# Performance work log

Hardware: AMD Instinct MI355X
Metric: run time of the kernel (lower is better)

The kernel has to match this reference:

```python
import jax, jax.numpy as jnp
import numpy as np

N = 50000
E = 800000
F_IN = 128
H = 128
M = 256


def setup_inputs() -> dict:
    key = jax.random.key(0)
    ks = jax.random.split(key, 12)
    x = jax.random.normal(ks[0], (N, F_IN), dtype=jnp.float32)
    edge_index = jax.random.randint(ks[1], (2, E), 0, N, dtype=jnp.int64)

    def glorot(k, shape):
        fan_in, fan_out = shape
        s = jnp.sqrt(6.0 / (fan_in + fan_out)).astype(jnp.float32)
        return jax.random.uniform(k, shape, jnp.float32, -s, s)

    return {
        "x": x,
        "edge_index": edge_index,
        # SAGEConv1: lin_l (neighbor aggregate, with bias), lin_r (root, no bias)
        "W1l": glorot(ks[2], (F_IN, H)), "b1l": jnp.zeros((H,), jnp.float32),
        "W1r": glorot(ks[3], (F_IN, H)),
        # SAGEConv2
        "W2l": glorot(ks[4], (H, H)), "b2l": jnp.zeros((H,), jnp.float32),
        "W2r": glorot(ks[5], (H, H)),
        # edge MLP: Linear(2H -> M), ReLU, Linear(M -> 1)
        "W3": glorot(ks[6], (2 * H, M)), "b3": jnp.zeros((M,), jnp.float32),
        "W4": glorot(ks[7], (M, 1)), "b4": jnp.zeros((1,), jnp.float32),
    }


def _sage_conv(x, src, dst, Wl, bl, Wr, num_nodes):
    # mean aggregation of source-node features at destination nodes
    agg = jax.ops.segment_sum(x[src], dst, num_segments=num_nodes)  # [N, F]
    cnt = jax.ops.segment_sum(jnp.ones((src.shape[0],), x.dtype), dst,
                              num_segments=num_nodes)
    agg = agg / jnp.maximum(cnt, 1.0)[:, None]
    # out = lin_l(agg) + lin_r(x)
    return agg @ Wl + bl + x @ Wr


def reference(x, edge_index, W1l, b1l, W1r, W2l, b2l, W2r, W3, b3, W4, b4):
    src, dst = edge_index[0], edge_index[1]
    h = jax.nn.relu(_sage_conv(x, src, dst, W1l, b1l, W1r, N))   # dropout: eval mode, identity
    h = jax.nn.relu(_sage_conv(h, src, dst, W2l, b2l, W2r, N))
    edge_feat = jnp.concatenate([h[src], h[dst]], axis=-1)       # [E, 2H]
    hidden = jax.nn.relu(edge_feat @ W3 + b3)                    # [E, M]
    pred = hidden @ W4 + b4                                      # [E, 1]
    return pred.reshape(-1)
```

## Files before the change

kernel.cpp:

```cpp
#include <hip/hip_runtime.h>
#include <hip/hip_bf16.h>

#define NN 50000
#define NE 800000
#define SCAN_G ((NN + 255) / 256)

typedef __attribute__((ext_vector_type(8))) short short8;
typedef __attribute__((ext_vector_type(4))) float f32x4;

__device__ inline float bf_lo(unsigned u) { u <<= 16; float f; __builtin_memcpy(&f, &u, 4); return f; }
__device__ inline float bf_hi(unsigned u) { u &= 0xffff0000u; float f; __builtin_memcpy(&f, &u, 4); return f; }
__device__ inline unsigned pack_bf16x2(float a, float b) {
    __hip_bfloat16 ba = __float2bfloat16(a), bb = __float2bfloat16(b);
    unsigned short ua, ub;
    __builtin_memcpy(&ua, &ba, 2);
    __builtin_memcpy(&ub, &bb, 2);
    return (unsigned)ua | ((unsigned)ub << 16);
}
__device__ inline __hip_bfloat16 f2bf(float a) { return __float2bfloat16(a); }

__global__ __launch_bounds__(256) void prep_all(const float* __restrict__ W3,
                                                __hip_bfloat16* __restrict__ wpq,
                                                const float* __restrict__ W1l,
                                                const float* __restrict__ W1r,
                                                const float* __restrict__ W2l,
                                                const float* __restrict__ W2r,
                                                __hip_bfloat16* __restrict__ w12t,
                                                int* __restrict__ cnt) {
    const int b = blockIdx.x;
    if (b < SCAN_G) {
        const int i = b * 256 + threadIdx.x;
        if (i < NN) cnt[i] = 0;
    } else if (b < SCAN_G + 64) {
        const int idx4 = ((b - SCAN_G) * 256 + threadIdx.x) * 4;
        const int c = idx4 >> 7;
        const int k0 = idx4 & 127;
#pragma unroll
        for (int i = 0; i < 4; ++i) {
            const int k = k0 + i;
            const float v = (c < 256) ? W3[k * 256 + c] : W3[(128 + k) * 256 + (c - 256)];
            wpq[c * 128 + k] = __float2bfloat16(v);
        }
    } else {
        const int idx = (b - SCAN_G - 64) * 256 + threadIdx.x;
        const int layer = idx >> 15;
        const int c = (idx >> 7) & 255;
        const int k = idx & 127;
        const float* W = layer ? (c < 128 ? W2l : W2r) : (c < 128 ? W1l : W1r);
        w12t[idx] = __float2bfloat16(W[k * 128 + (c & 127)]);
    }
}

__global__ __launch_bounds__(256) void hist_kernel(const int* __restrict__ ei,
                                                   int* __restrict__ cnt) {
    for (int e = blockIdx.x * 256 + threadIdx.x; e < NE; e += gridDim.x * 256)
        atomicAdd(&cnt[ei[NE + e]], 1);
}

__global__ __launch_bounds__(256) void scan_blk(const int* __restrict__ cnt,
                                                int* __restrict__ off,
                                                int* __restrict__ bsum) {
    __shared__ int sm[256];
    const int t = threadIdx.x;
    const int i = blockIdx.x * 256 + t;
    const int v = (i < NN) ? cnt[i] : 0;
    sm[t] = v;
    __syncthreads();
    for (int d = 1; d < 256; d <<= 1) {
        const int add = (t >= d) ? sm[t - d] : 0;
        __syncthreads();
        sm[t] += add;
        __syncthreads();
    }
    if (i < NN) off[i] = sm[t] - v;
    if (t == 255) bsum[blockIdx.x] = sm[255];
}

__global__ __launch_bounds__(256) void scan_add(int* __restrict__ off,
                                                int* __restrict__ cursor,
                                                const int* __restrict__ bsum) {
    __shared__ int red[256];
    const int t = threadIdx.x;
    int s = 0;
    for (int j = t; j < blockIdx.x; j += 256) s += bsum[j];
    red[t] = s;
    __syncthreads();
    for (int d = 128; d; d >>= 1) {
        if (t < d) red[t] += red[t + d];
        __syncthreads();
    }
    const int base = red[0];
    const int i = blockIdx.x * 256 + t;
    if (i < NN) {
        const int v = off[i] + base;
        off[i] = v;
        cursor[i] = v;
    }
    if (i == NN - 1) off[NN] = NE;
}

__global__ __launch_bounds__(256) void fill_kernel(const int* __restrict__ ei,
                                                   int* __restrict__ cursor,
                                                   int* __restrict__ ssrc,
                                                   int2* __restrict__ sde) {
    for (int e = blockIdx.x * 256 + threadIdx.x; e < NE; e += gridDim.x * 256) {
        const int d = ei[NE + e];
        const int p = atomicAdd(&cursor[d], 1);
        ssrc[p] = ei[e];
        sde[p] = make_int2(d, e);
    }
}

template <bool IN_F32>
__global__ __launch_bounds__(256) void proj_gemm(const void* __restrict__ inp,
                                                 const __hip_bfloat16* __restrict__ wt,
                                                 __hip_bfloat16* __restrict__ ob) {
    __shared__ __align__(16) char A[16384];
    const int t = threadIdx.x;
    const int n0 = blockIdx.x * 64;
    {
        const int row = t >> 2, part = t & 3;
        const int node = n0 + row;
        const int sw = (row & 7) << 4;
        if (IN_F32) {
            const float* xp = (const float*)inp + (size_t)node * 128 + part * 32;
#pragma unroll
            for (int i = 0; i < 8; ++i) {
                uint2 w = make_uint2(0u, 0u);
                if (node < NN) {
                    const float4 v = *(const float4*)(xp + i * 4);
                    w.x = pack_bf16x2(v.x, v.y);
                    w.y = pack_bf16x2(v.z, v.w);
                }
                const int inner = part * 64 + i * 8;
                *(uint2*)(A + row * 256 + (inner ^ sw)) = w;
            }
        } else {
            const char* srcp = (const char*)((const __hip_bfloat16*)inp + (size_t)node * 128);
#pragma unroll
            for (int i = 0; i < 4; ++i) {
                const int inner = part * 64 + i * 16;
                uint4 v = make_uint4(0u, 0u, 0u, 0u);
                if (node < NN) v = *(const uint4*)(srcp + inner);
                *(uint4*)(A + row * 256 + (inner ^ sw)) = v;
            }
        }
    }
    __syncthreads();

    const int w = t >> 6, l = t & 63;
    const int lr = l & 15, lg = l >> 4;
    const int cb = w * 64;
    f32x4 acc[4][4] = {};
    for (int ks = 0; ks < 4; ++ks) {
        short8 af[4], bf[4];
        const int innerA = ks * 64 + lg * 16;
#pragma unroll
        for (int rt = 0; rt < 4; ++rt) {
            const int row = rt * 16 + lr;
            af[rt] = *(const short8*)(A + row * 256 + (innerA ^ ((row & 7) << 4)));
        }
        const int kidx = ks * 32 + lg * 8;
#pragma unroll
        for (int ct = 0; ct < 4; ++ct) {
            const int col = cb + ct * 16 + lr;
            bf[ct] = *(const short8*)(wt + col * 128 + kidx);
        }
#pragma unroll
        for (int rt = 0; rt < 4; ++rt)
#pragma unroll
            for (int ct = 0; ct < 4; ++ct)
                acc[rt][ct] = __builtin_amdgcn_mfma_f32_16x16x32_bf16(af[rt], bf[ct], acc[rt][ct], 0, 0, 0);
    }
#pragma unroll
    for (int rt = 0; rt < 4; ++rt) {
        __syncthreads();
#pragma unroll
        for (int ct = 0; ct < 4; ++ct) {
            const int col = cb + ct * 16 + lr;
#pragma unroll
            for (int j = 0; j < 4; ++j) {
                const int row = lg * 4 + j;
                *(__hip_bfloat16*)(A + row * 528 + col * 2) = f2bf(acc[rt][ct][j]);
            }
        }
        __syncthreads();
        const int row = t >> 4, cc = t & 15;
        const int node = n0 + rt * 16 + row;
        if (node < NN) {
#pragma unroll
            for (int pass = 0; pass < 2; ++pass) {
                const int byteoff = pass * 256 + cc * 16;
                *(uint4*)((char*)(ob + (size_t)node * 256) + byteoff) =
                    *(const uint4*)(A + row * 528 + byteoff);
            }
        }
    }
}

__global__ __launch_bounds__(256) void gather_fuse(const __hip_bfloat16* __restrict__ ob,
                                                   const int* __restrict__ off,
                                                   const int* __restrict__ ssrc,
                                                   const float* __restrict__ bl,
                                                   __hip_bfloat16* __restrict__ outp) {
    const int wv = threadIdx.x >> 6, lane = threadIdx.x & 63;
    const float2 bv = *(const float2*)&bl[lane * 2];
    for (int n = blockIdx.x * 4 + wv; n < NN; n += gridDim.x * 4) {
        const int b = off[n], e = off[n + 1];
        float a0 = 0.f, a1 = 0.f;
        int i = b;
        int s0 = (i + 0 < e) ? ssrc[i + 0] : 0;
        int s1 = (i + 1 < e) ? ssrc[i + 1] : 0;
        int s2 = (i + 2 < e) ? ssrc[i + 2] : 0;
        int s3 = (i + 3 < e) ? ssrc[i + 3] : 0;
        for (; i + 4 <= e;) {
            const unsigned u0 = *(const unsigned*)(ob + (size_t)s0 * 256 + lane * 2);
            const unsigned u1 = *(const unsigned*)(ob + (size_t)s1 * 256 + lane * 2);
            const unsigned u2 = *(const unsigned*)(ob + (size_t)s2 * 256 + lane * 2);
            const unsigned u3 = *(const unsigned*)(ob + (size_t)s3 * 256 + lane * 2);
            i += 4;
            s0 = (i + 0 < e) ? ssrc[i + 0] : 0;
            s1 = (i + 1 < e) ? ssrc[i + 1] : 0;
            s2 = (i + 2 < e) ? ssrc[i + 2] : 0;
            s3 = (i + 3 < e) ? ssrc[i + 3] : 0;
            a0 += bf_lo(u0) + bf_lo(u1) + bf_lo(u2) + bf_lo(u3);
            a1 += bf_hi(u0) + bf_hi(u1) + bf_hi(u2) + bf_hi(u3);
        }
        if (i < e) {
            const unsigned u = *(const unsigned*)(ob + (size_t)s0 * 256 + lane * 2);
            a0 += bf_lo(u); a1 += bf_hi(u); ++i;
            if (i < e) {
                const unsigned u1_ = *(const unsigned*)(ob + (size_t)s1 * 256 + lane * 2);
                a0 += bf_lo(u1_); a1 += bf_hi(u1_); ++i;
                if (i < e) {
                    const unsigned u2_ = *(const unsigned*)(ob + (size_t)s2 * 256 + lane * 2);
                    a0 += bf_lo(u2_); a1 += bf_hi(u2_);
                }
            }
        }
        const float inv = 1.0f / fmaxf((float)(e - b), 1.0f);
        const unsigned uz = *(const unsigned*)(ob + (size_t)n * 256 + 128 + lane * 2);
        const float h0 = fmaxf(a0 * inv + bf_lo(uz) + bv.x, 0.0f);
        const float h1 = fmaxf(a1 * inv + bf_hi(uz) + bv.y, 0.0f);
        *(unsigned*)((char*)outp + (size_t)n * 256 + lane * 4) = pack_bf16x2(h0, h1);
    }
}

__global__ __launch_bounds__(256) void pq_gemm(const __hip_bfloat16* __restrict__ h2b,
                                               const __hip_bfloat16* __restrict__ wpq,
                                               const float* __restrict__ b3,
                                               __hip_bfloat16* __restrict__ pqb) {
    __shared__ __align__(16) char A[16640];
    const int t = threadIdx.x;
    const int n0 = blockIdx.x * 64;
    {
        const int row = t >> 2, part = t & 3;
        const int node = n0 + row;
        const int sw = (row & 7) << 4;
#pragma unroll
        for (int i = 0; i < 4; ++i) {
            const int inner = part * 64 + i * 16;
            uint4 v = make_uint4(0u, 0u, 0u, 0u);
            if (node < NN) v = *(const uint4*)((const char*)(h2b + node * 128) + inner);
            *(uint4*)(A + row * 256 + (inner ^ sw)) = v;
        }
    }
    __syncthreads();

    const int w = t >> 6, l = t & 63;
    const int lr = l & 15, lg = l >> 4;
    const int cb = w * 128;
    f32x4 acc[4][8] = {};
    for (int ks = 0; ks < 4; ++ks) {
        short8 af[4], bf[8];
        const int innerA = ks * 64 + lg * 16;
#pragma unroll
        for (int rt = 0; rt < 4; ++rt) {
            const int row = rt * 16 + lr;
            af[rt] = *(const short8*)(A + row * 256 + (innerA ^ ((row & 7) << 4)));
        }
        const int kidx = ks * 32 + lg * 8;
#pragma unroll
        for (int ct = 0; ct < 8; ++ct) {
            const int col = cb + ct * 16 + lr;
            bf[ct] = *(const short8*)(wpq + col * 128 + kidx);
        }
#pragma unroll
        for (int rt = 0; rt < 4; ++rt)
#pragma unroll
            for (int ct = 0; ct < 8; ++ct)
                acc[rt][ct] = __builtin_amdgcn_mfma_f32_16x16x32_bf16(af[rt], bf[ct], acc[rt][ct], 0, 0, 0);
    }
    float badd[8];
#pragma unroll
    for (int ct = 0; ct < 8; ++ct) {
        const int col = cb + ct * 16 + lr;
        badd[ct] = (col >= 256) ? b3[col - 256] : 0.f;
    }
#pragma unroll
    for (int rt = 0; rt < 4; ++rt) {
        __syncthreads();
#pragma unroll
        for (int ct = 0; ct < 8; ++ct) {
            const int col = cb + ct * 16 + lr;
#pragma unroll
            for (int j = 0; j < 4; ++j) {
                const int row = lg * 4 + j;
                *(__hip_bfloat16*)(A + row * 1040 + col * 2) = f2bf(acc[rt][ct][j] + badd[ct]);
            }
        }
        __syncthreads();
        const int row = t >> 4, cc = t & 15;
        const int node = n0 + rt * 16 + row;
        if (node < NN) {
#pragma unroll
            for (int pass = 0; pass < 4; ++pass) {
                const int byteoff = pass * 256 + cc * 16;
                *(uint4*)((char*)(pqb + (size_t)node * 512) + byteoff) =
                    *(const uint4*)(A + row * 1040 + byteoff);
            }
        }
    }
}

__global__ __launch_bounds__(256) void edge_kernel(const int* __restrict__ ssrc,
                                                   const int2* __restrict__ sde,
                                                   const __hip_bfloat16* __restrict__ pqb,
                                                   const float* __restrict__ W4,
                                                   const float* __restrict__ b4,
                                                   float* __restrict__ out) {
    const int i = threadIdx.x & 7;
    const int g = threadIdx.x >> 3;
    float w4r[4][8];
#pragma unroll
    for (int j = 0; j < 4; ++j)
#pragma unroll
        for (int u = 0; u < 8; ++u)
            w4r[j][u] = W4[i * 8 + j * 64 + u];
    const float b4v = b4[0];
    for (int p = blockIdx.x * 64 + g * 2; p < NE; p += gridDim.x * 64) {
        const int s0 = ssrc[p], s1 = ssrc[p + 1];
        const int2 de0 = sde[p], de1 = sde[p + 1];
        const char* P0 = (const char*)(pqb + (size_t)s0 * 512 + i * 8);
        const char* Q0 = (const char*)(pqb + (size_t)de0.x * 512 + 256 + i * 8);
        const char* P1 = (const char*)(pqb + (size_t)s1 * 512 + i * 8);
        const char* Q1 = (const char*)(pqb + (size_t)de1.x * 512 + 256 + i * 8);
        uint4 pv0[4], qv0[4], pv1[4], qv1[4];
#pragma unroll
        for (int j = 0; j < 4; ++j) {
            pv0[j] = *(const uint4*)(P0 + j * 128);
            qv0[j] = *(const uint4*)(Q0 + j * 128);
            pv1[j] = *(const uint4*)(P1 + j * 128);
            qv1[j] = *(const uint4*)(Q1 + j * 128);
        }
        float acc0 = 0.f, acc1 = 0.f;
#pragma unroll
        for (int j = 0; j < 4; ++j) {
            const unsigned pa0[4] = {pv0[j].x, pv0[j].y, pv0[j].z, pv0[j].w};
            const unsigned qa0[4] = {qv0[j].x, qv0[j].y, qv0[j].z, qv0[j].w};
            const unsigned pa1[4] = {pv1[j].x, pv1[j].y, pv1[j].z, pv1[j].w};
            const unsigned qa1[4] = {qv1[j].x, qv1[j].y, qv1[j].z, qv1[j].w};
#pragma unroll
            for (int q4 = 0; q4 < 4; ++q4) {
                const float h0l = fmaxf(bf_lo(pa0[q4]) + bf_lo(qa0[q4]), 0.f);
                const float h0h = fmaxf(bf_hi(pa0[q4]) + bf_hi(qa0[q4]), 0.f);
                acc0 = fmaf(h0l, w4r[j][q4 * 2], acc0);
                acc0 = fmaf(h0h, w4r[j][q4 * 2 + 1], acc0);
                const float h1l = fmaxf(bf_lo(pa1[q4]) + bf_lo(qa1[q4]), 0.f);
                const float h1h = fmaxf(bf_hi(pa1[q4]) + bf_hi(qa1[q4]), 0.f);
                acc1 = fmaf(h1l, w4r[j][q4 * 2], acc1);
                acc1 = fmaf(h1h, w4r[j][q4 * 2 + 1], acc1);
            }
        }
#pragma unroll
        for (int m = 1; m <= 4; m <<= 1) {
            acc0 += __shfl_xor(acc0, m);
            acc1 += __shfl_xor(acc1, m);
        }
        if (i == 0) {
            out[de0.y] = acc0 + b4v;
            out[de1.y] = acc1 + b4v;
        }
    }
}

extern "C" void kernel_launch(void* const* d_in, const int* in_sizes, int n_in,
                              void* d_out, int out_size, void* d_ws, size_t ws_size,
                              hipStream_t stream) {
    const float* x   = (const float*)d_in[0];
    const int* ei    = (const int*)d_in[1];
    const float* W1l = (const float*)d_in[2];
    const float* b1l = (const float*)d_in[3];
    const float* W1r = (const float*)d_in[4];
    const float* W2l = (const float*)d_in[5];
    const float* b2l = (const float*)d_in[6];
    const float* W2r = (const float*)d_in[7];
    const float* W3  = (const float*)d_in[8];
    const float* b3  = (const float*)d_in[9];
    const float* W4  = (const float*)d_in[10];
    const float* b4  = (const float*)d_in[11];
    float* out = (float*)d_out;

    char* ws = (char*)d_ws;
    int* cnt            = (int*)(ws);
    int* off            = (int*)(ws + 200704);
    int* cursor         = (int*)(ws + 401408);
    int* bsum           = cursor + NN;
    int* ssrc           = (int*)(ws + 602112);
    int2* sde           = (int2*)(ws + 3802112);
    __hip_bfloat16* pqb = (__hip_bfloat16*)(ws + 10202112);
    __hip_bfloat16* h1b = (__hip_bfloat16*)(ws + 23002112);
    __hip_bfloat16* ob  = (__hip_bfloat16*)(ws + 35802112);
    __hip_bfloat16* h2b = (__hip_bfloat16*)(ws + 61402112);
    __hip_bfloat16* wpq = (__hip_bfloat16*)(ws + 74202112);
    __hip_bfloat16* w12t= (__hip_bfloat16*)(ws + 74333184);

    prep_all<<<SCAN_G + 64 + 256, 256, 0, stream>>>(W3, wpq, W1l, W1r, W2l, W2r, w12t, cnt);
    hist_kernel<<<1024, 256, 0, stream>>>(ei, cnt);
    scan_blk<<<SCAN_G, 256, 0, stream>>>(cnt, off, bsum);
    scan_add<<<SCAN_G, 256, 0, stream>>>(off, cursor, bsum);
    fill_kernel<<<1024, 256, 0, stream>>>(ei, cursor, ssrc, sde);

    proj_gemm<true><<<(NN + 63) / 64, 256, 0, stream>>>((const void*)x, w12t, ob);
    gather_fuse<<<2048, 256, 0, stream>>>(ob, off, ssrc, b1l, h1b);
    proj_gemm<false><<<(NN + 63) / 64, 256, 0, stream>>>((const void*)h1b, w12t + 256 * 128, ob);
    gather_fuse<<<2048, 256, 0, stream>>>(ob, off, ssrc, b2l, h2b);
    pq_gemm<<<(NN + 63) / 64, 256, 0, stream>>>(h2b, wpq, b3, pqb);
    edge_kernel<<<2048, 256, 0, stream>>>(ssrc, sde, pqb, W4, b4, out);
}
```

Baseline: 396.2 us.

## Fuse layer-1 neighbor gather with layer-2 projection GEMM

Adds a fused kernel that performs the mean-aggregation gather, bias, root add and ReLU for layer 1, writes the resulting bf16 rows directly into shared memory, and then runs the layer-2 projection MFMA GEMM in the same block. This removes the h1 intermediate write and read and one kernel launch. In exchange the gather now runs with only 782 blocks of 64 nodes each instead of a grid-stride 2048-block launch, which may reduce latency hiding for the irregular gathers. Workspace buffers are re-assigned, and pqb aliases ob1, which is safe because ob1 is dead by then.

Measured after the change: 441.5 us. 11.4% more time.

```diff
diff --git a/kernel.cpp b/kernel.cpp
--- a/kernel.cpp
+++ b/kernel.cpp
@@ -111,8 +111,7 @@
     }
 }
 
-template <bool IN_F32>
-__global__ __launch_bounds__(256) void proj_gemm(const void* __restrict__ inp,
+__global__ __launch_bounds__(256) void proj_gemm(const float* __restrict__ inp,
                                                  const __hip_bfloat16* __restrict__ wt,
                                                  __hip_bfloat16* __restrict__ ob) {
     __shared__ __align__(16) char A[16384];
@@ -122,28 +121,17 @@
         const int row = t >> 2, part = t & 3;
         const int node = n0 + row;
         const int sw = (row & 7) << 4;
-        if (IN_F32) {
-            const float* xp = (const float*)inp + (size_t)node * 128 + part * 32;
-#pragma unroll
-            for (int i = 0; i < 8; ++i) {
-                uint2 w = make_uint2(0u, 0u);
-                if (node < NN) {
-                    const float4 v = *(const float4*)(xp + i * 4);
-                    w.x = pack_bf16x2(v.x, v.y);
-                    w.y = pack_bf16x2(v.z, v.w);
-                }
-                const int inner = part * 64 + i * 8;
-                *(uint2*)(A + row * 256 + (inner ^ sw)) = w;
-            }
-        } else {
-            const char* srcp = (const char*)((const __hip_bfloat16*)inp + (size_t)node * 128);
-#pragma unroll
-            for (int i = 0; i < 4; ++i) {
-                const int inner = part * 64 + i * 16;
-                uint4 v = make_uint4(0u, 0u, 0u, 0u);
-                if (node < NN) v = *(const uint4*)(srcp + inner);
-                *(uint4*)(A + row * 256 + (inner ^ sw)) = v;
-            }
+        const float* xp = inp + (size_t)node * 128 + part * 32;
+#pragma unroll
+        for (int i = 0; i < 8; ++i) {
+            uint2 w = make_uint2(0u, 0u);
+            if (node < NN) {
+                const float4 v = *(const float4*)(xp + i * 4);
+                w.x = pack_bf16x2(v.x, v.y);
+                w.y = pack_bf16x2(v.z, v.w);
+            }
+            const int inner = part * 64 + i * 8;
+            *(uint2*)(A + row * 256 + (inner ^ sw)) = w;
         }
     }
     __syncthreads();
@@ -192,6 +180,115 @@
             for (int pass = 0; pass < 2; ++pass) {
                 const int byteoff = pass * 256 + cc * 16;
                 *(uint4*)((char*)(ob + (size_t)node * 256) + byteoff) =
+                    *(const uint4*)(A + row * 528 + byteoff);
+            }
+        }
+    }
+}
+
+__global__ __launch_bounds__(256) void fused_gp(const __hip_bfloat16* __restrict__ ob_in,
+                                                const int* __restrict__ off,
+                                                const int* __restrict__ ssrc,
+                                                const float* __restrict__ bl,
+                                                const __hip_bfloat16* __restrict__ wt,
+                                                __hip_bfloat16* __restrict__ ob_out) {
+    __shared__ __align__(16) char A[16384];
+    const int t = threadIdx.x;
+    const int n0 = blockIdx.x * 64;
+    const int wv = t >> 6, lane = t & 63;
+    const float2 bv = *(const float2*)&bl[lane * 2];
+    for (int u = 0; u < 16; ++u) {
+        const int row = wv * 16 + u;
+        const int n = n0 + row;
+        unsigned hpack = 0u;
+        if (n < NN) {
+            const int b = off[n], e = off[n + 1];
+            float a0 = 0.f, a1 = 0.f;
+            int i = b;
+            int s0 = (i + 0 < e) ? ssrc[i + 0] : 0;
+            int s1 = (i + 1 < e) ? ssrc[i + 1] : 0;
+            int s2 = (i + 2 < e) ? ssrc[i + 2] : 0;
+            int s3 = (i + 3 < e) ? ssrc[i + 3] : 0;
+            for (; i + 4 <= e;) {
+                const unsigned u0 = *(const unsigned*)(ob_in + (size_t)s0 * 256 + lane * 2);
+                const unsigned u1 = *(const unsigned*)(ob_in + (size_t)s1 * 256 + lane * 2);
+                const unsigned u2 = *(const unsigned*)(ob_in + (size_t)s2 * 256 + lane * 2);
+                const unsigned u3 = *(const unsigned*)(ob_in + (size_t)s3 * 256 + lane * 2);
+                i += 4;
+                s0 = (i + 0 < e) ? ssrc[i + 0] : 0;
+                s1 = (i + 1 < e) ? ssrc[i + 1] : 0;
+                s2 = (i + 2 < e) ? ssrc[i + 2] : 0;
+                s3 = (i + 3 < e) ? ssrc[i + 3] : 0;
+                a0 += bf_lo(u0) + bf_lo(u1) + bf_lo(u2) + bf_lo(u3);
+                a1 += bf_hi(u0) + bf_hi(u1) + bf_hi(u2) + bf_hi(u3);
+            }
+            if (i < e) {
+                const unsigned uu = *(const unsigned*)(ob_in + (size_t)s0 * 256 + lane * 2);
+                a0 += bf_lo(uu); a1 += bf_hi(uu); ++i;
+                if (i < e) {
+                    const unsigned u1_ = *(const unsigned*)(ob_in + (size_t)s1 * 256 + lane * 2);
+                    a0 += bf_lo(u1_); a1 += bf_hi(u1_); ++i;
+                    if (i < e) {
+                        const unsigned u2_ = *(const unsigned*)(ob_in + (size_t)s2 * 256 + lane * 2);
+                        a0 += bf_lo(u2_); a1 += bf_hi(u2_);
+                    }
+                }
+            }
+            const float inv = 1.0f / fmaxf((float)(e - b), 1.0f);
+            const unsigned uz = *(const unsigned*)(ob_in + (size_t)n * 256 + 128 + lane * 2);
+            const float h0 = fmaxf(a0 * inv + bf_lo(uz) + bv.x, 0.0f);
+            const float h1 = fmaxf(a1 * inv + bf_hi(uz) + bv.y, 0.0f);
+            hpack = pack_bf16x2(h0, h1);
+        }
+        const int inner = lane * 4;
+        *(unsigned*)(A + row * 256 + (inner ^ ((row & 7) << 4))) = hpack;
+    }
+    __syncthreads();
+
+    const int w = t >> 6, l = t & 63;
+    const int lr = l & 15, lg = l >> 4;
+    const int cb = w * 64;
+    f32x4 acc[4][4] = {};
+    for (int ks = 0; ks < 4; ++ks) {
+        short8 af[4], bf[4];
+        const int innerA = ks * 64 + lg * 16;
+#pragma unroll
+        for (int rt = 0; rt < 4; ++rt) {
+            const int row = rt * 16 + lr;
+            af[rt] = *(const short8*)(A + row * 256 + (innerA ^ ((row & 7) << 4)));
+        }
+        const int kidx = ks * 32 + lg * 8;
+#pragma unroll
+        for (int ct = 0; ct < 4; ++ct) {
+            const int col = cb + ct * 16 + lr;
+            bf[ct] = *(const short8*)(wt + col * 128 + kidx);
+        }
+#pragma unroll
+        for (int rt = 0; rt < 4; ++rt)
+#pragma unroll
+            for (int ct = 0; ct < 4; ++ct)
+                acc[rt][ct] = __builtin_amdgcn_mfma_f32_16x16x32_bf16(af[rt], bf[ct], acc[rt][ct], 0, 0, 0);
+    }
+#pragma unroll
+    for (int rt = 0; rt < 4; ++rt) {
+        __syncthreads();
+#pragma unroll
+        for (int ct = 0; ct < 4; ++ct) {
+            const int col = cb + ct * 16 + lr;
+#pragma unroll
+            for (int j = 0; j < 4; ++j) {
+                const int row = lg * 4 + j;
+                *(__hip_bfloat16*)(A + row * 528 + col * 2) = f2bf(acc[rt][ct][j]);
+            }
+        }
+        __syncthreads();
+        const int row = t >> 4, cc = t & 15;
+        const int node = n0 + rt * 16 + row;
+        if (node < NN) {
+#pragma unroll
+            for (int pass = 0; pass < 2; ++pass) {
+                const int byteoff = pass * 256 + cc * 16;
+                *(uint4*)((char*)(ob_out + (size_t)node * 256) + byteoff) =
                     *(const uint4*)(A + row * 528 + byteoff);
             }
         }
@@ -408,10 +505,10 @@
     int* bsum           = cursor + NN;
     int* ssrc           = (int*)(ws + 602112);
     int2* sde           = (int2*)(ws + 3802112);
+    __hip_bfloat16* ob1 = (__hip_bfloat16*)(ws + 10202112);
+    __hip_bfloat16* ob2 = (__hip_bfloat16*)(ws + 35802112);
+    __hip_bfloat16* h2b = (__hip_bfloat16*)(ws + 61402112);
     __hip_bfloat16* pqb = (__hip_bfloat16*)(ws + 10202112);
-    __hip_bfloat16* h1b = (__hip_bfloat16*)(ws + 23002112);
-    __hip_bfloat16* ob  = (__hip_bfloat16*)(ws + 35802112);
-    __hip_bfloat16* h2b = (__hip_bfloat16*)(ws + 61402112);
     __hip_bfloat16* wpq = (__hip_bfloat16*)(ws + 74202112);
     __hip_bfloat16* w12t= (__hip_bfloat16*)(ws + 74333184);
 
@@ -421,10 +518,9 @@
     scan_add<<<SCAN_G, 256, 0, stream>>>(off, cursor, bsum);
     fill_kernel<<<1024, 256, 0, stream>>>(ei, cursor, ssrc, sde);
 
-    proj_gemm<true><<<(NN + 63) / 64, 256, 0, stream>>>((const void*)x, w12t, ob);
-    gather_fuse<<<2048, 256, 0, stream>>>(ob, off, ssrc, b1l, h1b);
-    proj_gemm<false><<<(NN + 63) / 64, 256, 0, stream>>>((const void*)h1b, w12t + 256 * 128, ob);
-    gather_fuse<<<2048, 256, 0, stream>>>(ob, off, ssrc, b2l, h2b);
+    proj_gemm<<<(NN + 63) / 64, 256, 0, stream>>>(x, w12t, ob1);
+    fused_gp<<<(NN + 63) / 64, 256, 0, stream>>>(ob1, off, ssrc, b1l, w12t + 256 * 128, ob2);
+    gather_fuse<<<2048, 256, 0, stream>>>(ob2, off, ssrc, b2l, h2b);
     pq_gemm<<<(NN + 63) / 64, 256, 0, stream>>>(h2b, wpq, b3, pqb);
     edge_kernel<<<2048, 256, 0, stream>>>(ssrc, sde, pqb, W4, b4, out);
 }
```

## Iterate edge kernel per destination node and merge CSR arrays into int2

Applied to the files above, without the earlier changes.

The edge kernel now walks the CSR by destination node, loads the node's Q half of the projection once, and streams over its incoming edges with a one-ahead software prefetch of the source P rows. This cuts the per-edge Q reload. The separate ssrc and sde arrays are merged into one int2 (src, edge id) array, which lowers the write traffic in fill_kernel. The cost is that gather_fuse now reads 8-byte entries to get the source index, and the per-node loop brings load imbalance from varying degree plus a serial dependency across edges.

Result: no change. 399.6 us (+0.9%).

```diff
diff --git a/kernel.cpp b/kernel.cpp
--- a/kernel.cpp
+++ b/kernel.cpp
@@ -101,13 +101,11 @@
 
 __global__ __launch_bounds__(256) void fill_kernel(const int* __restrict__ ei,
                                                    int* __restrict__ cursor,
-                                                   int* __restrict__ ssrc,
-                                                   int2* __restrict__ sde) {
+                                                   int2* __restrict__ ssei) {
     for (int e = blockIdx.x * 256 + threadIdx.x; e < NE; e += gridDim.x * 256) {
         const int d = ei[NE + e];
         const int p = atomicAdd(&cursor[d], 1);
-        ssrc[p] = ei[e];
-        sde[p] = make_int2(d, e);
+        ssei[p] = make_int2(ei[e], e);
     }
 }
 
@@ -200,7 +198,7 @@
 
 __global__ __launch_bounds__(256) void gather_fuse(const __hip_bfloat16* __restrict__ ob,
                                                    const int* __restrict__ off,
-                                                   const int* __restrict__ ssrc,
+                                                   const int2* __restrict__ ssei,
                                                    const float* __restrict__ bl,
                                                    __hip_bfloat16* __restrict__ outp) {
     const int wv = threadIdx.x >> 6, lane = threadIdx.x & 63;
@@ -209,20 +207,20 @@
         const int b = off[n], e = off[n + 1];
         float a0 = 0.f, a1 = 0.f;
         int i = b;
-        int s0 = (i + 0 < e) ? ssrc[i + 0] : 0;
-        int s1 = (i + 1 < e) ? ssrc[i + 1] : 0;
-        int s2 = (i + 2 < e) ? ssrc[i + 2] : 0;
-        int s3 = (i + 3 < e) ? ssrc[i + 3] : 0;
+        int s0 = (i + 0 < e) ? ssei[i + 0].x : 0;
+        int s1 = (i + 1 < e) ? ssei[i + 1].x : 0;
+        int s2 = (i + 2 < e) ? ssei[i + 2].x : 0;
+        int s3 = (i + 3 < e) ? ssei[i + 3].x : 0;
         for (; i + 4 <= e;) {
             const unsigned u0 = *(const unsigned*)(ob + (size_t)s0 * 256 + lane * 2);
             const unsigned u1 = *(const unsigned*)(ob + (size_t)s1 * 256 + lane * 2);
             const unsigned u2 = *(const unsigned*)(ob + (size_t)s2 * 256 + lane * 2);
             const unsigned u3 = *(const unsigned*)(ob + (size_t)s3 * 256 + lane * 2);
             i += 4;
-            s0 = (i + 0 < e) ? ssrc[i + 0] : 0;
-            s1 = (i + 1 < e) ? ssrc[i + 1] : 0;
-            s2 = (i + 2 < e) ? ssrc[i + 2] : 0;
-            s3 = (i + 3 < e) ? ssrc[i + 3] : 0;
+            s0 = (i + 0 < e) ? ssei[i + 0].x : 0;
+            s1 = (i + 1 < e) ? ssei[i + 1].x : 0;
+            s2 = (i + 2 < e) ? ssei[i + 2].x : 0;
+            s3 = (i + 3 < e) ? ssei[i + 3].x : 0;
             a0 += bf_lo(u0) + bf_lo(u1) + bf_lo(u2) + bf_lo(u3);
             a1 += bf_hi(u0) + bf_hi(u1) + bf_hi(u2) + bf_hi(u3);
         }
@@ -323,8 +321,8 @@
     }
 }
 
-__global__ __launch_bounds__(256) void edge_kernel(const int* __restrict__ ssrc,
-                                                   const int2* __restrict__ sde,
+__global__ __launch_bounds__(256) void edge_kernel(const int* __restrict__ off,
+                                                   const int2* __restrict__ ssei,
                                                    const __hip_bfloat16* __restrict__ pqb,
                                                    const float* __restrict__ W4,
                                                    const float* __restrict__ b4,
@@ -338,48 +336,49 @@
         for (int u = 0; u < 8; ++u)
             w4r[j][u] = W4[i * 8 + j * 64 + u];
     const float b4v = b4[0];
-    for (int p = blockIdx.x * 64 + g * 2; p < NE; p += gridDim.x * 64) {
-        const int s0 = ssrc[p], s1 = ssrc[p + 1];
-        const int2 de0 = sde[p], de1 = sde[p + 1];
-        const char* P0 = (const char*)(pqb + (size_t)s0 * 512 + i * 8);
-        const char* Q0 = (const char*)(pqb + (size_t)de0.x * 512 + 256 + i * 8);
-        const char* P1 = (const char*)(pqb + (size_t)s1 * 512 + i * 8);
-        const char* Q1 = (const char*)(pqb + (size_t)de1.x * 512 + 256 + i * 8);
-        uint4 pv0[4], qv0[4], pv1[4], qv1[4];
-#pragma unroll
-        for (int j = 0; j < 4; ++j) {
-            pv0[j] = *(const uint4*)(P0 + j * 128);
-            qv0[j] = *(const uint4*)(Q0 + j * 128);
-            pv1[j] = *(const uint4*)(P1 + j * 128);
-            qv1[j] = *(const uint4*)(Q1 + j * 128);
-        }
-        float acc0 = 0.f, acc1 = 0.f;
-#pragma unroll
-        for (int j = 0; j < 4; ++j) {
-            const unsigned pa0[4] = {pv0[j].x, pv0[j].y, pv0[j].z, pv0[j].w};
-            const unsigned qa0[4] = {qv0[j].x, qv0[j].y, qv0[j].z, qv0[j].w};
-            const unsigned pa1[4] = {pv1[j].x, pv1[j].y, pv1[j].z, pv1[j].w};
-            const unsigned qa1[4] = {qv1[j].x, qv1[j].y, qv1[j].z, qv1[j].w};
-#pragma unroll
-            for (int q4 = 0; q4 < 4; ++q4) {
-                const float h0l = fmaxf(bf_lo(pa0[q4]) + bf_lo(qa0[q4]), 0.f);
-                const float h0h = fmaxf(bf_hi(pa0[q4]) + bf_hi(qa0[q4]), 0.f);
-                acc0 = fmaf(h0l, w4r[j][q4 * 2], acc0);
-                acc0 = fmaf(h0h, w4r[j][q4 * 2 + 1], acc0);
-                const float h1l = fmaxf(bf_lo(pa1[q4]) + bf_lo(qa1[q4]), 0.f);
-                const float h1h = fmaxf(bf_hi(pa1[q4]) + bf_hi(qa1[q4]), 0.f);
-                acc1 = fmaf(h1l, w4r[j][q4 * 2], acc1);
-                acc1 = fmaf(h1h, w4r[j][q4 * 2 + 1], acc1);
-            }
-        }
-#pragma unroll
-        for (int m = 1; m <= 4; m <<= 1) {
-            acc0 += __shfl_xor(acc0, m);
-            acc1 += __shfl_xor(acc1, m);
-        }
-        if (i == 0) {
-            out[de0.y] = acc0 + b4v;
-            out[de1.y] = acc1 + b4v;
+    for (int n = blockIdx.x * 32 + g; n < NN; n += gridDim.x * 32) {
+        const int b = off[n], e = off[n + 1];
+        if (b == e) continue;
+        const char* Qp = (const char*)(pqb + (size_t)n * 512 + 256 + i * 8);
+        uint4 qv[4];
+#pragma unroll
+        for (int j = 0; j < 4; ++j) qv[j] = *(const uint4*)(Qp + j * 128);
+        int2 cur = ssei[b];
+        uint4 pv[4];
+        {
+            const char* Pp = (const char*)(pqb + (size_t)cur.x * 512 + i * 8);
+#pragma unroll
+            for (int j = 0; j < 4; ++j) pv[j] = *(const uint4*)(Pp + j * 128);
+        }
+        for (int p = b; p < e; ++p) {
+            int2 nxt = cur;
+            uint4 pn[4] = {pv[0], pv[1], pv[2], pv[3]};
+            if (p + 1 < e) {
+                nxt = ssei[p + 1];
+                const char* Pp = (const char*)(pqb + (size_t)nxt.x * 512 + i * 8);
+#pragma unroll
+                for (int j = 0; j < 4; ++j) pn[j] = *(const uint4*)(Pp + j * 128);
+            }
+            float acc = 0.f;
+#pragma unroll
+            for (int j = 0; j < 4; ++j) {
+                const unsigned pa[4] = {pv[j].x, pv[j].y, pv[j].z, pv[j].w};
+                const unsigned qa[4] = {qv[j].x, qv[j].y, qv[j].z, qv[j].w};
+#pragma unroll
+                for (int q4 = 0; q4 < 4; ++q4) {
+                    const float hlo = fmaxf(bf_lo(pa[q4]) + bf_lo(qa[q4]), 0.f);
+                    const float hhi = fmaxf(bf_hi(pa[q4]) + bf_hi(qa[q4]), 0.f);
+                    acc = fmaf(hlo, w4r[j][q4 * 2], acc);
+                    acc = fmaf(hhi, w4r[j][q4 * 2 + 1], acc);
+                }
+            }
+            acc += __shfl_xor(acc, 1);
+            acc += __shfl_xor(acc, 2);
+            acc += __shfl_xor(acc, 4);
+            if (i == 0) out[cur.y] = acc + b4v;
+            cur = nxt;
+#pragma unroll
+            for (int j = 0; j < 4; ++j) pv[j] = pn[j];
         }
     }
 }
@@ -406,8 +405,7 @@
     int* off            = (int*)(ws + 200704);
     int* cursor         = (int*)(ws + 401408);
     int* bsum           = cursor + NN;
-    int* ssrc           = (int*)(ws + 602112);
-    int2* sde           = (int2*)(ws + 3802112);
+    int2* ssei          = (int2*)(ws + 602112);
     __hip_bfloat16* pqb = (__hip_bfloat16*)(ws + 10202112);
     __hip_bfloat16* h1b = (__hip_bfloat16*)(ws + 23002112);
     __hip_bfloat16* ob  = (__hip_bfloat16*)(ws + 35802112);
@@ -419,12 +417,12 @@
     hist_kernel<<<1024, 256, 0, stream>>>(ei, cnt);
     scan_blk<<<SCAN_G, 256, 0, stream>>>(cnt, off, bsum);
     scan_add<<<SCAN_G, 256, 0, stream>>>(off, cursor, bsum);
-    fill_kernel<<<1024, 256, 0, stream>>>(ei, cursor, ssrc, sde);
+    fill_kernel<<<1024, 256, 0, stream>>>(ei, cursor, ssei);
 
     proj_gemm<true><<<(NN + 63) / 64, 256, 0, stream>>>((const void*)x, w12t, ob);
-    gather_fuse<<<2048, 256, 0, stream>>>(ob, off, ssrc, b1l, h1b);
+    gather_fuse<<<2048, 256, 0, stream>>>(ob, off, ssei, b1l, h1b);
     proj_gemm<false><<<(NN + 63) / 64, 256, 0, stream>>>((const void*)h1b, w12t + 256 * 128, ob);
-    gather_fuse<<<2048, 256, 0, stream>>>(ob, off, ssrc, b2l, h2b);
+    gather_fuse<<<2048, 256, 0, stream>>>(ob, off, ssei, b2l, h2b);
     pq_gemm<<<(NN + 63) / 64, 256, 0, stream>>>(h2b, wpq, b3, pqb);
-    edge_kernel<<<2048, 256, 0, stream>>>(ssrc, sde, pqb, W4, b4, out);
-}
+    edge_kernel<<<2048, 256, 0, stream>>>(off, ssei, pqb, W4, b4, out);
+}
```
